# Optimization experiments

Measured on AMD Instinct MI355X. Metric: run time of the kernel, lower is better.

Reference implementation:

```python
import jax, jax.numpy as jnp
import numpy as np

N, E, R = 50000, 640000, 3
EMB, HID, NCLS, G = 64, 128, 4, 512
NSHAPE, NCOLOR = 16, 16
IN_DIM = 2 * EMB + 1


def setup_inputs() -> dict:
    key = jax.random.key(0)
    ks = jax.random.split(key, 16)
    gl = lambda k, shp, fan: (jax.random.normal(k, shp, jnp.float32) / np.sqrt(fan)).astype(jnp.float32)
    return {
        "pos": jax.random.normal(ks[0], (N, 1), jnp.float32),
        "shape_id": jax.random.randint(ks[1], (N,), 0, NSHAPE),
        "color_id": jax.random.randint(ks[2], (N,), 0, NCOLOR),
        "edge_index": jax.random.randint(ks[3], (2, E), 0, N),
        "edge_type": jax.random.randint(ks[4], (E,), 0, R),
        "batch": jnp.sort(jax.random.randint(ks[5], (N,), 0, G)),
        "shape_emb_w": jax.random.normal(ks[6], (NSHAPE, EMB), jnp.float32),
        "color_emb_w": jax.random.normal(ks[7], (NCOLOR, EMB), jnp.float32),
        "W1": gl(ks[8], (R, IN_DIM, HID), IN_DIM),
        "root1": gl(ks[9], (IN_DIM, HID), IN_DIM),
        "b1": jnp.zeros((HID,), jnp.float32),
        "W2": gl(ks[10], (R, HID, HID), HID),
        "root2": gl(ks[11], (HID, HID), HID),
        "b2": jnp.zeros((HID,), jnp.float32),
        "lin_w": gl(ks[12], (HID, NCLS), HID),
        "lin_b": jnp.zeros((NCLS,), jnp.float32),
    }


def rgcn_conv(x, edge_index, edge_type, W, root, b):
    """PyG RGCNConv: per-relation mean aggregation of source features,
    then per-relation linear, summed; plus root transform and bias."""
    n = x.shape[0]
    src, dst = edge_index[0], edge_index[1]
    seg = edge_type * n + dst                          # [E] relation-major segment id
    msg = x[src]                                       # [E, d] gather
    sums = jax.ops.segment_sum(msg, seg, num_segments=R * n).reshape(R, n, -1)
    cnt = jax.ops.segment_sum(jnp.ones((E,), x.dtype), seg, num_segments=R * n).reshape(R, n, 1)
    mean = sums / jnp.maximum(cnt, 1.0)                # [R, n, d]
    return jnp.einsum('rnd,rdh->nh', mean, W) + x @ root + b


def reference(pos, shape_id, color_id, edge_index, edge_type, batch,
              shape_emb_w, color_emb_w, W1, root1, b1, W2, root2, b2, lin_w, lin_b):
    x = jnp.concatenate([shape_emb_w[shape_id], color_emb_w[color_id], pos], axis=1)  # [N, IN_DIM]
    x = jax.nn.relu(rgcn_conv(x, edge_index, edge_type, W1, root1, b1))
    # dropout is identity at inference
    x = jax.nn.relu(rgcn_conv(x, edge_index, edge_type, W2, root2, b2))
    # global mean pool per graph
    s = jax.ops.segment_sum(x, batch, num_segments=G)
    c = jax.ops.segment_sum(jnp.ones((x.shape[0],), x.dtype), batch, num_segments=G)[:, None]
    pooled = s / jnp.maximum(c, 1.0)                   # [G, HID]
    return pooled @ lin_w + lin_b                      # [G, NCLS]
```

## Files before the change

### kernel.cpp

```cpp
#include <hip/hip_runtime.h>
#include <hip/hip_bf16.h>

#define NNODE 50000
#define NEDGE 640000
#define NREL  3
#define HIDD  128
#define GNUM  512
#define K1M   128
#define K2    512
#define NB    196
#define EQ    (NEDGE / 4)
#define CNT_BLOCKS ((EQ + 255) / 256)
#define TAB_BLOCKS ((K1M * 128 + 33 * 128 + K2 * 128 + 255) / 256)

typedef float  f32x4   __attribute__((ext_vector_type(4)));
typedef short  vshort8 __attribute__((ext_vector_type(8)));

#define SWZ(row, kb) ((((kb) ^ (((row) >> 1) & 3)) << 3))

__device__ __forceinline__ short bf16_rne(float f) {
    unsigned u = __float_as_uint(f);
    return (short)((u + 0x7FFFu + ((u >> 16) & 1u)) >> 16);
}

__global__ void count_build_kernel(const int* __restrict__ ei, const int* __restrict__ et,
                                   const int* __restrict__ shape_id, const int* __restrict__ color_id,
                                   const float* __restrict__ pos,
                                   int* __restrict__ cnt, int* __restrict__ rank,
                                   int2* __restrict__ nf,
                                   const float* __restrict__ shape_w, const float* __restrict__ color_w,
                                   const float* __restrict__ W1, const float* __restrict__ root1,
                                   const float* __restrict__ W2, const float* __restrict__ root2,
                                   short* __restrict__ B1th, float* __restrict__ rootTab,
                                   short* __restrict__ Bt_hi) {
    if (blockIdx.x < CNT_BLOCKS) {
        int tid = blockIdx.x * blockDim.x + threadIdx.x;
        if (tid < NNODE) nf[tid] = make_int2(shape_id[tid] | (color_id[tid] << 8), __float_as_int(pos[tid]));
        if (tid >= EQ) return;
        int e0 = tid, e1 = tid + EQ, e2 = tid + 2 * EQ, e3 = tid + 3 * EQ;
        int d0 = ei[NEDGE + e0], d1 = ei[NEDGE + e1], d2 = ei[NEDGE + e2], d3 = ei[NEDGE + e3];
        int r0 = et[e0], r1 = et[e1], r2 = et[e2], r3 = et[e3];
        int k0 = atomicAdd(&cnt[d0 * 3 + r0], 1);
        int k1 = atomicAdd(&cnt[d1 * 3 + r1], 1);
        int k2 = atomicAdd(&cnt[d2 * 3 + r2], 1);
        int k3 = atomicAdd(&cnt[d3 * 3 + r3], 1);
        rank[e0] = k0; rank[e1] = k1; rank[e2] = k2; rank[e3] = k3;
        return;
    }
    int idx = (blockIdx.x - CNT_BLOCKS) * blockDim.x + threadIdx.x;
    if (idx < K1M * 128) {
        int k = idx >> 7, n = idx & 127;
        float v = 0.f;
        if (k < 99) {
            int r = k / 33, j = k - r * 33;
            const float* Wsrc = W1 + (size_t)r * 129 * 128;
            if (j < 16) {
                for (int e = 0; e < 64; ++e) v += shape_w[j * 64 + e] * Wsrc[e * 128 + n];
            } else if (j < 32) {
                int c = j - 16;
                for (int e = 0; e < 64; ++e) v += color_w[c * 64 + e] * Wsrc[(64 + e) * 128 + n];
            } else {
                v = Wsrc[128 * 128 + n];
            }
        }
        B1th[(size_t)n * K1M + k] = bf16_rne(v);
        return;
    }
    int idx2 = idx - K1M * 128;
    if (idx2 < 33 * 128) {
        int h = idx2 & 127, j = idx2 >> 7;
        float v;
        if (j < 16) {
            v = 0.f;
            for (int e = 0; e < 64; ++e) v += shape_w[j * 64 + e] * root1[e * 128 + h];
        } else if (j < 32) {
            int c = j - 16;
            v = 0.f;
            for (int e = 0; e < 64; ++e) v += color_w[c * 64 + e] * root1[(64 + e) * 128 + h];
        } else {
            v = root1[128 * 128 + h];
        }
        rootTab[j * 128 + h] = v;
        return;
    }
    int idx3 = idx2 - 33 * 128;
    if (idx3 >= K2 * 128) return;
    int k = idx3 >> 7, n = idx3 & 127;
    float v = (k < 384) ? W2[idx3] : root2[idx3 - 384 * 128];
    Bt_hi[(size_t)n * K2 + k] = bf16_rne(v);
}

__global__ void scan_partial_kernel(const int* __restrict__ cnt, int* __restrict__ partial,
                                    float* __restrict__ pooled) {
    __shared__ int sh[256];
    int t = threadIdx.x, i = blockIdx.x * 256 + t;
    for (int z = i; z < GNUM * 128; z += NB * 256) pooled[z] = 0.f;
    int v = (i < NNODE) ? cnt[3 * i] + cnt[3 * i + 1] + cnt[3 * i + 2] : 0;
    sh[t] = v; __syncthreads();
    for (int o = 128; o > 0; o >>= 1) { if (t < o) sh[t] += sh[t + o]; __syncthreads(); }
    if (t == 0) partial[blockIdx.x] = sh[0];
}

__global__ void scan_final_kernel(const int* __restrict__ cnt, const int* __restrict__ partial,
                                  int* __restrict__ offs3, float* __restrict__ rcnt) {
    __shared__ int shp[256];
    __shared__ int sh[256];
    int t = threadIdx.x, i = blockIdx.x * 256 + t;
    int pv = (t < NB) ? partial[t] : 0;
    shp[t] = pv; __syncthreads();
    for (int o = 1; o < 256; o <<= 1) {
        int x = (t >= o) ? shp[t - o] : 0; __syncthreads();
        shp[t] += x; __syncthreads();
    }
    int blockOff = (blockIdx.x > 0) ? shp[blockIdx.x - 1] : 0;
    int c0 = 0, c1 = 0, c2 = 0;
    if (i < NNODE) { c0 = cnt[3 * i]; c1 = cnt[3 * i + 1]; c2 = cnt[3 * i + 2]; }
    int v = c0 + c1 + c2;
    sh[t] = v; __syncthreads();
    for (int o = 1; o < 256; o <<= 1) {
        int x = (t >= o) ? sh[t - o] : 0; __syncthreads();
        sh[t] += x; __syncthreads();
    }
    int exc = sh[t] - v + blockOff;
    if (i < NNODE) {
        offs3[3 * i]     = exc;
        offs3[3 * i + 1] = exc + c0;
        offs3[3 * i + 2] = exc + c0 + c1;
        float4 rc = make_float4(1.f / fmaxf((float)c0, 1.f), 1.f / fmaxf((float)c1, 1.f),
                                1.f / fmaxf((float)c2, 1.f), 1.f);
        *(float4*)&rcnt[i * 4] = rc;
    }
    if (blockIdx.x == 0 && t == 0) offs3[3 * NNODE] = NEDGE;
}

__global__ void fill_kernel(const int* __restrict__ ei, const int* __restrict__ et,
                            const int* __restrict__ rank, const int* __restrict__ offs3,
                            int* __restrict__ sorted) {
    int tid = blockIdx.x * blockDim.x + threadIdx.x;
    if (tid >= EQ) return;
    int e0 = tid, e1 = tid + EQ, e2 = tid + 2 * EQ, e3 = tid + 3 * EQ;
    int s0 = ei[e0], s1 = ei[e1], s2 = ei[e2], s3 = ei[e3];
    int d0 = ei[NEDGE + e0], d1 = ei[NEDGE + e1], d2 = ei[NEDGE + e2], d3 = ei[NEDGE + e3];
    int r0 = et[e0], r1 = et[e1], r2 = et[e2], r3 = et[e3];
    int k0 = rank[e0], k1 = rank[e1], k2 = rank[e2], k3 = rank[e3];
    int p0 = offs3[d0 * 3 + r0] + k0;
    int p1 = offs3[d1 * 3 + r1] + k1;
    int p2 = offs3[d2 * 3 + r2] + k2;
    int p3 = offs3[d3 * 3 + r3] + k3;
    sorted[p0] = s0 | (r0 << 16);
    sorted[p1] = s1 | (r1 << 16);
    sorted[p2] = s2 | (r2 << 16);
    sorted[p3] = s3 | (r3 << 16);
}

__global__ __launch_bounds__(256) void hist1_kernel(const int* __restrict__ offs3,
                                                    const int* __restrict__ sorted,
                                                    const int2* __restrict__ nf,
                                                    const float* __restrict__ rcnt,
                                                    unsigned short* __restrict__ A1h) {
    __shared__ float hist[16][102];
    int t = threadIdx.x;
    int sub = t >> 4;
    int lane16 = t & 15;
    int d = blockIdx.x * 16 + sub;
    float* hf = hist[sub];
#pragma unroll
    for (int z = lane16; z < 102; z += 16) hf[z] = 0.f;
    if (d < NNODE) {
        int beg = offs3[3 * d], end = offs3[3 * d + 3];
        for (int i = beg + lane16; i < end; i += 16) {
            int w = sorted[i];
            int s = w & 0xFFFF, r = (w >> 16) & 3;
            int2 f = nf[s];
            atomicAdd(&hf[r * 34 + (f.x & 0xFF)], 1.f);
            atomicAdd(&hf[r * 34 + 16 + (f.x >> 8)], 1.f);
            atomicAdd(&hf[r * 34 + 32], __int_as_float(f.y));
        }
        float rc0 = rcnt[d * 4 + 0], rc1 = rcnt[d * 4 + 1], rc2 = rcnt[d * 4 + 2];
        vshort8 outv;
#pragma unroll
        for (int j = 0; j < 8; ++j) {
            int slot = lane16 * 8 + j;
            float v = 0.f;
            if (slot < 99) {
                int r = slot / 33;
                float rc = (r == 0) ? rc0 : ((r == 1) ? rc1 : rc2);
                v = hf[r * 34 + (slot - r * 33)] * rc;
            }
            outv[j] = bf16_rne(v);
        }
        *(vshort8*)&A1h[(size_t)d * K1M + lane16 * 8] = outv;
    }
}

__global__ __launch_bounds__(256) void aggregate_kernel(const int* __restrict__ offs3,
                                                        const int* __restrict__ sorted,
                                                        const float* __restrict__ rcnt,
                                                        unsigned short* __restrict__ A2h) {
    int lane = threadIdx.x & 63;
    int d = (blockIdx.x << 2) + (threadIdx.x >> 6);
    if (d >= NNODE) return;
    int b0  = __builtin_amdgcn_readfirstlane(offs3[3 * d]);
    int b1  = __builtin_amdgcn_readfirstlane(offs3[3 * d + 1]);
    int b2  = __builtin_amdgcn_readfirstlane(offs3[3 * d + 2]);
    int end = __builtin_amdgcn_readfirstlane(offs3[3 * d + 3]);
    const unsigned* xp = (const unsigned*)A2h;
    float a00 = 0.f, a01 = 0.f, a10 = 0.f, a11 = 0.f, a20 = 0.f, a21 = 0.f;
#define AGG_ACC(ii, x) {                                            \
        float lo_ = __uint_as_float((x) << 16);                     \
        float hi_ = __uint_as_float((x) & 0xFFFF0000u);             \
        if ((ii) >= b2)      { a20 += lo_; a21 += hi_; }            \
        else if ((ii) >= b1) { a10 += lo_; a11 += hi_; }            \
        else                 { a00 += lo_; a01 += hi_; } }
#define AGG_LD(j)  unsigned x##j = xp[((size_t)(unsigned)(sorted[i + j] & 0xFFFF) << 8) + 192 + lane]
    int i = b0;
    for (; i + 8 <= end; i += 8) {
        AGG_LD(0); AGG_LD(1); AGG_LD(2); AGG_LD(3);
        AGG_LD(4); AGG_LD(5); AGG_LD(6); AGG_LD(7);
        AGG_ACC(i, x0); AGG_ACC(i + 1, x1); AGG_ACC(i + 2, x2); AGG_ACC(i + 3, x3);
        AGG_ACC(i + 4, x4); AGG_ACC(i + 5, x5); AGG_ACC(i + 6, x6); AGG_ACC(i + 7, x7);
    }
    for (; i + 4 <= end; i += 4) {
        AGG_LD(0); AGG_LD(1); AGG_LD(2); AGG_LD(3);
        AGG_ACC(i, x0); AGG_ACC(i + 1, x1); AGG_ACC(i + 2, x2); AGG_ACC(i + 3, x3);
    }
    for (; i < end; ++i) {
        AGG_LD(0);
        AGG_ACC(i, x0);
    }
#undef AGG_LD
#undef AGG_ACC
    float rc0 = rcnt[d * 4 + 0], rc1 = rcnt[d * 4 + 1], rc2 = rcnt[d * 4 + 2];
    size_t base = (size_t)d * 512 + (lane << 1);
#define AGG_OUT(vA, vB, rel) {                                        \
        unsigned short h0_ = (unsigned short)bf16_rne(vA);            \
        unsigned short h1_ = (unsigned short)bf16_rne(vB);            \
        *(unsigned*)&A2h[base + (rel) * 128] = (unsigned)h0_ | ((unsigned)h1_ << 16); }
    AGG_OUT(a00 * rc0, a01 * rc0, 0);
    AGG_OUT(a10 * rc1, a11 * rc1, 1);
    AGG_OUT(a20 * rc2, a21 * rc2, 2);
#undef AGG_OUT
}

__global__ __launch_bounds__(256) void gemm1_mfma_kernel(
    const unsigned short* __restrict__ A1h,
    const short* __restrict__ B1th,
    const int* __restrict__ shape_id, const int* __restrict__ color_id,
    const float* __restrict__ pos, const float* __restrict__ rootTab,
    const float* __restrict__ bias,
    unsigned short* __restrict__ A2h) {
    __shared__ short Ah[64][32];
    __shared__ short Bh[128][32];
    const int t    = threadIdx.x;
    const int lane = t & 63;
    const int w    = t >> 6;
    const int wm   = w >> 1, wn = w & 1;
    const int bm0  = blockIdx.x * 64;
    const int lr   = lane & 15, lk = lane >> 4;
    const int sr = t >> 2, skb = t & 3;
    int gra = bm0 + sr; if (gra >= NNODE) gra = NNODE - 1;
    f32x4 acc[2][4] = {};
    for (int kt = 0; kt < K1M; kt += 32) {
        vshort8 avh = *(const vshort8*)&A1h[(size_t)gra * K1M + kt + skb * 8];
        vshort8 bvh0 = *(const vshort8*)&B1th[(size_t)sr * K1M + kt + skb * 8];
        vshort8 bvh1 = *(const vshort8*)&B1th[(size_t)(sr + 64) * K1M + kt + skb * 8];
        __syncthreads();
        *(vshort8*)&Ah[sr][SWZ(sr, skb)]           = avh;
        *(vshort8*)&Bh[sr][SWZ(sr, skb)]           = bvh0;
        *(vshort8*)&Bh[sr + 64][SWZ(sr + 64, skb)] = bvh1;
        __syncthreads();
        vshort8 afh[2], bfh[4];
#pragma unroll
        for (int mf = 0; mf < 2; ++mf) {
            int row = wm * 32 + mf * 16 + lr;
            afh[mf] = *(const vshort8*)&Ah[row][SWZ(row, lk)];
        }
#pragma unroll
        for (int nf2 = 0; nf2 < 4; ++nf2) {
            int row = wn * 64 + nf2 * 16 + lr;
            bfh[nf2] = *(const vshort8*)&Bh[row][SWZ(row, lk)];
        }
#pragma unroll
        for (int mf = 0; mf < 2; ++mf)
#pragma unroll
            for (int nf2 = 0; nf2 < 4; ++nf2)
                acc[mf][nf2] = __builtin_amdgcn_mfma_f32_16x16x32_bf16(afh[mf], bfh[nf2], acc[mf][nf2], 0, 0, 0);
    }
#pragma unroll
    for (int mf = 0; mf < 2; ++mf) {
        int mb = bm0 + wm * 32 + mf * 16 + (lane >> 4) * 4;
#pragma unroll
        for (int r = 0; r < 4; ++r) {
            int gm = mb + r;
            if (gm >= NNODE) continue;
            int sid = shape_id[gm], cid = color_id[gm];
            float pv = pos[gm];
#pragma unroll
            for (int nf2 = 0; nf2 < 4; ++nf2) {
                int n = wn * 64 + nf2 * 16 + lr;
                float v = acc[mf][nf2][r] + rootTab[sid * 128 + n] + rootTab[(16 + cid) * 128 + n]
                        + pv * rootTab[32 * 128 + n] + bias[n];
                A2h[(size_t)gm * 512 + 384 + n] = (unsigned short)bf16_rne(fmaxf(v, 0.f));
            }
        }
    }
}

__global__ __launch_bounds__(256) void gemm2_mfma_kernel(
    const unsigned short* __restrict__ A2h,
    const short* __restrict__ Bt_hi,
    const float* __restrict__ bias,
    const int* __restrict__ batch,
    float* __restrict__ pooled) {
    __shared__ char smem[64 * 132 * 4 + 256];
    short (*Ah)[32]   = (short(*)[32])smem;
    short (*Bh)[32]   = (short(*)[32])(smem + 4096);
    float (*Cst)[132] = (float(*)[132])smem;
    int*  batchLDS    = (int*)(smem + 64 * 132 * 4);
    const int t    = threadIdx.x;
    const int lane = t & 63;
    const int w    = t >> 6;
    const int wm   = w >> 1, wn = w & 1;
    const int bm0  = blockIdx.x * 64;
    const int lr   = lane & 15, lk = lane >> 4;
    const int sr = t >> 2, skb = t & 3;
    int gra = bm0 + sr; if (gra >= NNODE) gra = NNODE - 1;
    f32x4 acc[2][4] = {};
    for (int kt = 0; kt < K2; kt += 32) {
        vshort8 avh = *(const vshort8*)&A2h[(size_t)gra * K2 + kt + skb * 8];
        vshort8 bvh0 = *(const vshort8*)&Bt_hi[(size_t)sr * K2 + kt + skb * 8];
        vshort8 bvh1 = *(const vshort8*)&Bt_hi[(size_t)(sr + 64) * K2 + kt + skb * 8];
        __syncthreads();
        *(vshort8*)&Ah[sr][SWZ(sr, skb)]           = avh;
        *(vshort8*)&Bh[sr][SWZ(sr, skb)]           = bvh0;
        *(vshort8*)&Bh[sr + 64][SWZ(sr + 64, skb)] = bvh1;
        __syncthreads();
        vshort8 afh[2], bfh[4];
#pragma unroll
        for (int mf = 0; mf < 2; ++mf) {
            int row = wm * 32 + mf * 16 + lr;
            afh[mf] = *(const vshort8*)&Ah[row][SWZ(row, lk)];
        }
#pragma unroll
        for (int nf2 = 0; nf2 < 4; ++nf2) {
            int row = wn * 64 + nf2 * 16 + lr;
            bfh[nf2] = *(const vshort8*)&Bh[row][SWZ(row, lk)];
        }
#pragma unroll
        for (int mf = 0; mf < 2; ++mf)
#pragma unroll
            for (int nf2 = 0; nf2 < 4; ++nf2)
                acc[mf][nf2] = __builtin_amdgcn_mfma_f32_16x16x32_bf16(afh[mf], bfh[nf2], acc[mf][nf2], 0, 0, 0);
    }
    __syncthreads();
#pragma unroll
    for (int mf = 0; mf < 2; ++mf) {
        int rb = wm * 32 + mf * 16 + (lane >> 4) * 4;
#pragma unroll
        for (int nf2 = 0; nf2 < 4; ++nf2) {
            int n = wn * 64 + nf2 * 16 + lr;
            float bn = bias[n];
#pragma unroll
            for (int r = 0; r < 4; ++r)
                Cst[rb + r][n] = fmaxf(acc[mf][nf2][r] + bn, 0.f);
        }
    }
    if (t < 64) batchLDS[t] = (bm0 + t < NNODE) ? batch[bm0 + t] : -1;
    __syncthreads();
    {
        int col  = t & 127;
        int rbeg = (t >> 7) * 32;
        float accp = 0.f;
        int cur = batchLDS[rbeg];
        for (int rr = 0; rr < 32; ++rr) {
            int row = rbeg + rr;
            int g = batchLDS[row];
            if (g != cur) {
                if (cur >= 0) atomicAdd(&pooled[cur * 128 + col], accp);
                accp = 0.f; cur = g;
            }
            if (g >= 0) accp += Cst[row][col];
        }
        if (cur >= 0) atomicAdd(&pooled[cur * 128 + col], accp);
    }
}

__global__ void final_kernel(const float* __restrict__ pooled, const int* __restrict__ batch,
                             const float* __restrict__ lin_w, const float* __restrict__ lin_b,
                             float* __restrict__ out) {
    int idx = blockIdx.x * blockDim.x + threadIdx.x;
    if (idx >= GNUM * 4) return;
    int g = idx >> 2, c = idx & 3;
    int lo = 0, hi = NNODE;
    while (lo < hi) { int m = (lo + hi) >> 1; if (batch[m] < g) lo = m + 1; else hi = m; }
    int lo2 = lo, hi2 = NNODE;
    while (lo2 < hi2) { int m = (lo2 + hi2) >> 1; if (batch[m] < g + 1) lo2 = m + 1; else hi2 = m; }
    float cntf = (float)max(lo2 - lo, 1);
    float dot = 0.f;
    for (int k = 0; k < 128; ++k) dot += pooled[g * 128 + k] * lin_w[k * 4 + c];
    out[idx] = dot / cntf + lin_b[c];
}

extern "C" void kernel_launch(void* const* d_in, const int* in_sizes, int n_in,
                              void* d_out, int out_size, void* d_ws, size_t ws_size,
                              hipStream_t stream) {
    const float* pos      = (const float*)d_in[0];
    const int*   shape_id = (const int*)d_in[1];
    const int*   color_id = (const int*)d_in[2];
    const int*   ei       = (const int*)d_in[3];
    const int*   et       = (const int*)d_in[4];
    const int*   batch    = (const int*)d_in[5];
    const float* shape_w  = (const float*)d_in[6];
    const float* color_w  = (const float*)d_in[7];
    const float* W1       = (const float*)d_in[8];
    const float* root1    = (const float*)d_in[9];
    const float* b1       = (const float*)d_in[10];
    const float* W2       = (const float*)d_in[11];
    const float* root2    = (const float*)d_in[12];
    const float* b2       = (const float*)d_in[13];
    const float* lin_w    = (const float*)d_in[14];
    const float* lin_b    = (const float*)d_in[15];
    float* out = (float*)d_out;

    char* p = (char*)d_ws;
    auto alloc = [&](size_t bytes) { char* r = p; p += (bytes + 255) & ~(size_t)255; return r; };
    int*   cnt     = (int*)alloc((size_t)NNODE * 3 * 4);
    unsigned short* A1h = (unsigned short*)alloc((size_t)NNODE * K1M * 2);
    float* rcntBuf = (float*)alloc((size_t)NNODE * 4 * 4);
    unsigned short* A2h = (unsigned short*)alloc((size_t)NNODE * K2 * 2);
    float* rootTab = (float*)alloc((size_t)33 * 128 * 4);
    short* B1th    = (short*)alloc((size_t)128 * K1M * 2);
    short* Bt_hi   = (short*)alloc((size_t)128 * K2 * 2);
    float* pooled  = (float*)alloc((size_t)GNUM * 128 * 4);
    int2*  nfTab   = (int2*)alloc((size_t)NNODE * 8);
    int*   sorted  = (int*)alloc((size_t)NEDGE * 4);
    int*   offs3   = (int*)alloc((size_t)(3 * NNODE + 1) * 4);
    int*   rank    = (int*)alloc((size_t)NEDGE * 4);
    int*   partial = (int*)alloc((size_t)NB * 4);

    hipMemsetAsync(cnt, 0, (size_t)NNODE * 3 * 4, stream);

    count_build_kernel<<<CNT_BLOCKS + TAB_BLOCKS, 256, 0, stream>>>(
        ei, et, shape_id, color_id, pos, cnt, rank, nfTab,
        shape_w, color_w, W1, root1, W2, root2, B1th, rootTab, Bt_hi);

    scan_partial_kernel<<<NB, 256, 0, stream>>>(cnt, partial, pooled);
    scan_final_kernel<<<NB, 256, 0, stream>>>(cnt, partial, offs3, rcntBuf);
    fill_kernel<<<(EQ + 255) / 256, 256, 0, stream>>>(ei, et, rank, offs3, sorted);

    hist1_kernel<<<(NNODE + 15) / 16, 256, 0, stream>>>(offs3, sorted, nfTab, rcntBuf, A1h);

    gemm1_mfma_kernel<<<(NNODE + 63) / 64, 256, 0, stream>>>(
        A1h, B1th, shape_id, color_id, pos, rootTab, b1, A2h);

    aggregate_kernel<<<(NNODE + 3) / 4, 256, 0, stream>>>(offs3, sorted, rcntBuf, A2h);

    gemm2_mfma_kernel<<<(NNODE + 63) / 64, 256, 0, stream>>>(
        A2h, Bt_hi, b2, batch, pooled);

    final_kernel<<<(GNUM * 4 + 255) / 256, 256, 0, stream>>>(
        pooled, batch, lin_w, lin_b, out);
}
```

Baseline: 149.0 us.

## Fuse layer-2 neighbor aggregation into GEMM2 via LDS-resident A tile

Merges the aggregate kernel into the second GEMM. Each 64-row block now gathers and mean-aggregates its neighbor features straight into a 64x512 bf16 LDS tile, then runs the MFMA loop reading A from LDS. Layer-1 output goes to a compact 128-wide buffer, which shrinks the gather stride. This removes the global write and re-read of the 50000x512 A2 matrix and one kernel launch. In exchange each block needs about 72KB of LDS, which limits occupancy, and the gather runs with only 4 waves per block, each handling 16 rows serially.

```diff
diff --git a/kernel.cpp b/kernel.cpp
--- a/kernel.cpp
+++ b/kernel.cpp
@@ -193,62 +193,13 @@
     }
 }
 
-__global__ __launch_bounds__(256) void aggregate_kernel(const int* __restrict__ offs3,
-                                                        const int* __restrict__ sorted,
-                                                        const float* __restrict__ rcnt,
-                                                        unsigned short* __restrict__ A2h) {
-    int lane = threadIdx.x & 63;
-    int d = (blockIdx.x << 2) + (threadIdx.x >> 6);
-    if (d >= NNODE) return;
-    int b0  = __builtin_amdgcn_readfirstlane(offs3[3 * d]);
-    int b1  = __builtin_amdgcn_readfirstlane(offs3[3 * d + 1]);
-    int b2  = __builtin_amdgcn_readfirstlane(offs3[3 * d + 2]);
-    int end = __builtin_amdgcn_readfirstlane(offs3[3 * d + 3]);
-    const unsigned* xp = (const unsigned*)A2h;
-    float a00 = 0.f, a01 = 0.f, a10 = 0.f, a11 = 0.f, a20 = 0.f, a21 = 0.f;
-#define AGG_ACC(ii, x) {                                            \
-        float lo_ = __uint_as_float((x) << 16);                     \
-        float hi_ = __uint_as_float((x) & 0xFFFF0000u);             \
-        if ((ii) >= b2)      { a20 += lo_; a21 += hi_; }            \
-        else if ((ii) >= b1) { a10 += lo_; a11 += hi_; }            \
-        else                 { a00 += lo_; a01 += hi_; } }
-#define AGG_LD(j)  unsigned x##j = xp[((size_t)(unsigned)(sorted[i + j] & 0xFFFF) << 8) + 192 + lane]
-    int i = b0;
-    for (; i + 8 <= end; i += 8) {
-        AGG_LD(0); AGG_LD(1); AGG_LD(2); AGG_LD(3);
-        AGG_LD(4); AGG_LD(5); AGG_LD(6); AGG_LD(7);
-        AGG_ACC(i, x0); AGG_ACC(i + 1, x1); AGG_ACC(i + 2, x2); AGG_ACC(i + 3, x3);
-        AGG_ACC(i + 4, x4); AGG_ACC(i + 5, x5); AGG_ACC(i + 6, x6); AGG_ACC(i + 7, x7);
-    }
-    for (; i + 4 <= end; i += 4) {
-        AGG_LD(0); AGG_LD(1); AGG_LD(2); AGG_LD(3);
-        AGG_ACC(i, x0); AGG_ACC(i + 1, x1); AGG_ACC(i + 2, x2); AGG_ACC(i + 3, x3);
-    }
-    for (; i < end; ++i) {
-        AGG_LD(0);
-        AGG_ACC(i, x0);
-    }
-#undef AGG_LD
-#undef AGG_ACC
-    float rc0 = rcnt[d * 4 + 0], rc1 = rcnt[d * 4 + 1], rc2 = rcnt[d * 4 + 2];
-    size_t base = (size_t)d * 512 + (lane << 1);
-#define AGG_OUT(vA, vB, rel) {                                        \
-        unsigned short h0_ = (unsigned short)bf16_rne(vA);            \
-        unsigned short h1_ = (unsigned short)bf16_rne(vB);            \
-        *(unsigned*)&A2h[base + (rel) * 128] = (unsigned)h0_ | ((unsigned)h1_ << 16); }
-    AGG_OUT(a00 * rc0, a01 * rc0, 0);
-    AGG_OUT(a10 * rc1, a11 * rc1, 1);
-    AGG_OUT(a20 * rc2, a21 * rc2, 2);
-#undef AGG_OUT
-}
-
 __global__ __launch_bounds__(256) void gemm1_mfma_kernel(
     const unsigned short* __restrict__ A1h,
     const short* __restrict__ B1th,
     const int* __restrict__ shape_id, const int* __restrict__ color_id,
     const float* __restrict__ pos, const float* __restrict__ rootTab,
     const float* __restrict__ bias,
-    unsigned short* __restrict__ A2h) {
+    unsigned short* __restrict__ x1b) {
     __shared__ short Ah[64][32];
     __shared__ short Bh[128][32];
     const int t    = threadIdx.x;
@@ -300,38 +251,90 @@
                 int n = wn * 64 + nf2 * 16 + lr;
                 float v = acc[mf][nf2][r] + rootTab[sid * 128 + n] + rootTab[(16 + cid) * 128 + n]
                         + pv * rootTab[32 * 128 + n] + bias[n];
-                A2h[(size_t)gm * 512 + 384 + n] = (unsigned short)bf16_rne(fmaxf(v, 0.f));
+                x1b[(size_t)gm * 128 + n] = (unsigned short)bf16_rne(fmaxf(v, 0.f));
             }
         }
     }
 }
 
-__global__ __launch_bounds__(256) void gemm2_mfma_kernel(
-    const unsigned short* __restrict__ A2h,
-    const short* __restrict__ Bt_hi,
-    const float* __restrict__ bias,
-    const int* __restrict__ batch,
-    float* __restrict__ pooled) {
-    __shared__ char smem[64 * 132 * 4 + 256];
-    short (*Ah)[32]   = (short(*)[32])smem;
-    short (*Bh)[32]   = (short(*)[32])(smem + 4096);
+__global__ __launch_bounds__(256) void layer2_kernel(
+    const int* __restrict__ offs3, const int* __restrict__ sorted,
+    const float* __restrict__ rcnt, const unsigned short* __restrict__ x1b,
+    const short* __restrict__ Bt_hi, const float* __restrict__ bias,
+    const int* __restrict__ batch, float* __restrict__ pooled) {
+    __shared__ char smem[64 * 512 * 2 + 128 * 32 * 2 + 256];
+    short (*A2t)[512] = (short(*)[512])smem;
+    short (*Bh)[32]   = (short(*)[32])(smem + 65536);
+    int*  batchLDS    = (int*)(smem + 65536 + 8192);
     float (*Cst)[132] = (float(*)[132])smem;
-    int*  batchLDS    = (int*)(smem + 64 * 132 * 4);
     const int t    = threadIdx.x;
     const int lane = t & 63;
     const int w    = t >> 6;
     const int wm   = w >> 1, wn = w & 1;
     const int bm0  = blockIdx.x * 64;
     const int lr   = lane & 15, lk = lane >> 4;
+    const unsigned* xp = (const unsigned*)x1b;
+
+    for (int li = 0; li < 16; ++li) {
+        int row = w * 16 + li;
+        int d = bm0 + row;
+        if (d >= NNODE) break;
+        int b0  = __builtin_amdgcn_readfirstlane(offs3[3 * d]);
+        int b1  = __builtin_amdgcn_readfirstlane(offs3[3 * d + 1]);
+        int b2  = __builtin_amdgcn_readfirstlane(offs3[3 * d + 2]);
+        int end = __builtin_amdgcn_readfirstlane(offs3[3 * d + 3]);
+        float a00 = 0.f, a01 = 0.f, a10 = 0.f, a11 = 0.f, a20 = 0.f, a21 = 0.f;
+#define AGG_ACC(ii, x) {                                            \
+        float lo_ = __uint_as_float((x) << 16);                     \
+        float hi_ = __uint_as_float((x) & 0xFFFF0000u);             \
+        if ((ii) >= b2)      { a20 += lo_; a21 += hi_; }            \
+        else if ((ii) >= b1) { a10 += lo_; a11 += hi_; }            \
+        else                 { a00 += lo_; a01 += hi_; } }
+#define AGG_LD(j)  unsigned x##j = xp[((size_t)(unsigned)(sorted[i + j] & 0xFFFF) << 6) + lane]
+        int i = b0;
+        for (; i + 8 <= end; i += 8) {
+            AGG_LD(0); AGG_LD(1); AGG_LD(2); AGG_LD(3);
+            AGG_LD(4); AGG_LD(5); AGG_LD(6); AGG_LD(7);
+            AGG_ACC(i, x0); AGG_ACC(i + 1, x1); AGG_ACC(i + 2, x2); AGG_ACC(i + 3, x3);
+            AGG_ACC(i + 4, x4); AGG_ACC(i + 5, x5); AGG_ACC(i + 6, x6); AGG_ACC(i + 7, x7);
+        }
+        for (; i + 4 <= end; i += 4) {
+            AGG_LD(0); AGG_LD(1); AGG_LD(2); AGG_LD(3);
+            AGG_ACC(i, x0); AGG_ACC(i + 1, x1); AGG_ACC(i + 2, x2); AGG_ACC(i + 3, x3);
+        }
+        for (; i < end; ++i) {
+            AGG_LD(0);
+            AGG_ACC(i, x0);
+        }
+#undef AGG_LD
+#undef AGG_ACC
+        float rc0 = rcnt[d * 4 + 0], rc1 = rcnt[d * 4 + 1], rc2 = rcnt[d * 4 + 2];
+#define AGG_ST(vA, vB, rel) {                                                 \
+        int col0 = (rel) * 128 + (lane << 1);                                 \
+        int phys = ((col0 >> 5) << 5) + SWZ(row, (col0 >> 3) & 3) + (col0 & 7); \
+        unsigned short h0_ = (unsigned short)bf16_rne(vA);                    \
+        unsigned short h1_ = (unsigned short)bf16_rne(vB);                    \
+        *(unsigned*)&A2t[row][phys] = (unsigned)h0_ | ((unsigned)h1_ << 16); }
+        AGG_ST(a00 * rc0, a01 * rc0, 0);
+        AGG_ST(a10 * rc1, a11 * rc1, 1);
+        AGG_ST(a20 * rc2, a21 * rc2, 2);
+#undef AGG_ST
+    }
+    {
+        int row = t >> 2, q = t & 3;
+        int grow = bm0 + row; if (grow >= NNODE) grow = NNODE - 1;
+#pragma unroll
+        for (int kb = 0; kb < 4; ++kb) {
+            vshort8 v = *(const vshort8*)&x1b[(size_t)grow * 128 + q * 32 + kb * 8];
+            *(vshort8*)&A2t[row][(12 + q) * 32 + SWZ(row, kb)] = v;
+        }
+    }
     const int sr = t >> 2, skb = t & 3;
-    int gra = bm0 + sr; if (gra >= NNODE) gra = NNODE - 1;
     f32x4 acc[2][4] = {};
     for (int kt = 0; kt < K2; kt += 32) {
-        vshort8 avh = *(const vshort8*)&A2h[(size_t)gra * K2 + kt + skb * 8];
         vshort8 bvh0 = *(const vshort8*)&Bt_hi[(size_t)sr * K2 + kt + skb * 8];
         vshort8 bvh1 = *(const vshort8*)&Bt_hi[(size_t)(sr + 64) * K2 + kt + skb * 8];
         __syncthreads();
-        *(vshort8*)&Ah[sr][SWZ(sr, skb)]           = avh;
         *(vshort8*)&Bh[sr][SWZ(sr, skb)]           = bvh0;
         *(vshort8*)&Bh[sr + 64][SWZ(sr + 64, skb)] = bvh1;
         __syncthreads();
@@ -339,7 +342,7 @@
 #pragma unroll
         for (int mf = 0; mf < 2; ++mf) {
             int row = wm * 32 + mf * 16 + lr;
-            afh[mf] = *(const vshort8*)&Ah[row][SWZ(row, lk)];
+            afh[mf] = *(const vshort8*)&A2t[row][kt + SWZ(row, lk)];
         }
 #pragma unroll
         for (int nf2 = 0; nf2 < 4; ++nf2) {
@@ -427,7 +430,7 @@
     int*   cnt     = (int*)alloc((size_t)NNODE * 3 * 4);
     unsigned short* A1h = (unsigned short*)alloc((size_t)NNODE * K1M * 2);
     float* rcntBuf = (float*)alloc((size_t)NNODE * 4 * 4);
-    unsigned short* A2h = (unsigned short*)alloc((size_t)NNODE * K2 * 2);
+    unsigned short* x1b = (unsigned short*)alloc((size_t)NNODE * 128 * 2);
     float* rootTab = (float*)alloc((size_t)33 * 128 * 4);
     short* B1th    = (short*)alloc((size_t)128 * K1M * 2);
     short* Bt_hi   = (short*)alloc((size_t)128 * K2 * 2);
@@ -451,12 +454,10 @@
     hist1_kernel<<<(NNODE + 15) / 16, 256, 0, stream>>>(offs3, sorted, nfTab, rcntBuf, A1h);
 
     gemm1_mfma_kernel<<<(NNODE + 63) / 64, 256, 0, stream>>>(
-        A1h, B1th, shape_id, color_id, pos, rootTab, b1, A2h);
-
-    aggregate_kernel<<<(NNODE + 3) / 4, 256, 0, stream>>>(offs3, sorted, rcntBuf, A2h);
-
-    gemm2_mfma_kernel<<<(NNODE + 63) / 64, 256, 0, stream>>>(
-        A2h, Bt_hi, b2, batch, pooled);
+        A1h, B1th, shape_id, color_id, pos, rootTab, b1, x1b);
+
+    layer2_kernel<<<(NNODE + 63) / 64, 256, 0, stream>>>(
+        offs3, sorted, rcntBuf, x1b, Bt_hi, b2, batch, pooled);
 
     final_kernel<<<(GNUM * 4 + 255) / 256, 256, 0, stream>>>(
         pooled, batch, lin_w, lin_b, out);
```

Result: slower. 204.7 us (+37.4%).
